# Performance work log

Hardware: AMD Instinct MI355X
Metric: run time of the kernel (lower is better)

Reference implementation:

```python
import jax, jax.numpy as jnp
import numpy as np

N_HEAD = 16
N_KV_HEAD = 4
HEAD_DIM = 64
ROPE_THETA = 10000.0
EPS = 1e-6


def _rope_cos_sin(T, D, theta):
    # matches torch: freqs_cis[t, i] = exp(1j * t * theta**(-2i/D)), i in [0, D//2)
    inv_freq = theta ** (-jnp.arange(0, D, 2, dtype=jnp.float32) / D)  # [D//2]
    freqs = jnp.arange(T, dtype=jnp.float32)[:, None] * inv_freq[None, :]  # [T, D//2]
    return jnp.cos(freqs), jnp.sin(freqs)


def _apply_rope(x, cos, sin):
    # x: [B, T, H, D]; pairs are (even, odd) along last dim, complex-multiplied by freqs_cis
    B, T, H, D = x.shape
    xr = x.reshape(B, T, H, D // 2, 2)
    xe, xo = xr[..., 0], xr[..., 1]
    c = cos[None, :, None, :]  # [1, T, 1, D//2]
    s = sin[None, :, None, :]
    oe = xe * c - xo * s
    oo = xe * s + xo * c
    return jnp.stack([oe, oo], axis=-1).reshape(B, T, H, D)


def _qk_norm(x):
    rms = jnp.sqrt(jnp.mean(x * x, axis=-1, keepdims=True) + EPS)
    return x / rms


def setup_inputs() -> dict:
    key = jax.random.key(0)
    k = jax.random.split(key, 5)
    B, T, C = 4, 2048, 1024
    sc = 1.0 / np.sqrt(C)
    return {
        "x": jax.random.normal(k[0], (B, T, C), jnp.float32),
        "wq": jax.random.normal(k[1], (N_HEAD * HEAD_DIM, C), jnp.float32) * sc,
        "wk": jax.random.normal(k[2], (N_KV_HEAD * HEAD_DIM, C), jnp.float32) * sc,
        "wv": jax.random.normal(k[3], (N_KV_HEAD * HEAD_DIM, C), jnp.float32) * sc,
        "wo": jax.random.normal(k[4], (C, N_HEAD * HEAD_DIM), jnp.float32) * sc,
    }


def reference(x, wq, wk, wv, wo):
    B, T, C = x.shape
    H, KVH, D = N_HEAD, N_KV_HEAD, HEAD_DIM
    n_rep = H // KVH

    q = (x @ wq.T).reshape(B, T, H, D)
    k = (x @ wk.T).reshape(B, T, KVH, D)
    v = (x @ wv.T).reshape(B, T, KVH, D)

    cos, sin = _rope_cos_sin(T, D, ROPE_THETA)
    q = _qk_norm(_apply_rope(q, cos, sin))
    k = _qk_norm(_apply_rope(k, cos, sin))

    # GQA expand kv heads to n_head
    k = jnp.repeat(k, n_rep, axis=2)  # [B, T, H, D]
    v = jnp.repeat(v, n_rep, axis=2)

    q = q.transpose(0, 2, 1, 3)  # [B, H, T, D]
    k = k.transpose(0, 2, 1, 3)
    v = v.transpose(0, 2, 1, 3)

    scale = 1.0 / np.sqrt(D)
    scores = jnp.einsum("bhqd,bhkd->bhqk", q, k) * scale
    causal = jnp.tril(jnp.ones((T, T), dtype=bool))
    scores = jnp.where(causal[None, None], scores, -jnp.inf)
    attn = jax.nn.softmax(scores, axis=-1)
    y = jnp.einsum("bhqk,bhkd->bhqd", attn, v)  # [B, H, T, D]
    y = y.transpose(0, 2, 1, 3).reshape(B, T, H * D)
    return y @ wo.T
```

## Files before the change

kernel.cpp:

```cpp
#include <hip/hip_runtime.h>
#include <hip/hip_bf16.h>
#include <type_traits>

typedef __attribute__((ext_vector_type(8))) __bf16 bf16x8;
typedef __attribute__((ext_vector_type(2))) float f32x2;
typedef __attribute__((ext_vector_type(4))) float f32x4;
typedef __attribute__((ext_vector_type(16))) float f32x16;

#define MFMA16(a, b, c) __builtin_amdgcn_mfma_f32_16x16x32_bf16((a), (b), (c), 0, 0, 0)
#define MFMA32(a, b, c) __builtin_amdgcn_mfma_f32_32x32x16_bf16((a), (b), (c), 0, 0, 0)

__device__ __forceinline__ unsigned short f2bf(float f) {
    unsigned u = __builtin_bit_cast(unsigned, f);
    u = (u + 0x7fffu + ((u >> 16) & 1u)) >> 16;
    return (unsigned short)u;
}

__device__ __forceinline__ float bf2f(unsigned short u) {
    return __builtin_bit_cast(float, (unsigned)u << 16);
}

__device__ __forceinline__ unsigned cvt_pk_bf16(float lo, float hi) {
    unsigned r;
    asm("v_cvt_pk_bf16_f32 %0, %1, %2" : "=v"(r) : "v"(lo), "v"(hi));
    return r;
}

__device__ __forceinline__ void permswap(unsigned& a, unsigned& b) {
    asm("v_permlane32_swap_b32 %0, %1" : "+v"(a), "+v"(b));
}

__device__ __forceinline__ void gll16(const void* g, void* l) {
    __builtin_amdgcn_global_load_lds((const __attribute__((address_space(1))) void*)g,
                                     (__attribute__((address_space(3))) void*)l, 16, 0, 0);
}

__global__ __launch_bounds__(256) void cvt_fused(const float4* __restrict__ x,
                                                 const float4* __restrict__ wq,
                                                 const float4* __restrict__ wk,
                                                 const float4* __restrict__ wv,
                                                 const float4* __restrict__ wo,
                                                 ushort4* __restrict__ xb,
                                                 ushort4* __restrict__ wqkvb,
                                                 ushort4* __restrict__ wob,
                                                 float2* __restrict__ tbl) {
    int i = blockIdx.x * 256 + threadIdx.x;
    if (i < 2752512) {
        const float4* src; ushort4* dst; int j;
        if (i < 2097152)      { src = x;  dst = xb;             j = i; }
        else if (i < 2359296) { src = wq; dst = wqkvb;          j = i - 2097152; }
        else if (i < 2424832) { src = wk; dst = wqkvb + 262144; j = i - 2359296; }
        else if (i < 2490368) { src = wv; dst = wqkvb + 327680; j = i - 2424832; }
        else                  { src = wo; dst = wob;            j = i - 2490368; }
        float4 v = src[j];
        ushort4 o;
        o.x = f2bf(v.x); o.y = f2bf(v.y); o.z = f2bf(v.z); o.w = f2bf(v.w);
        dst[j] = o;
    } else {
        int j = i - 2752512;
        int t = j >> 5, k = j & 31;
        float inv = powf(10000.0f, -(float)(2 * k) * (1.0f / 64.0f));
        float a = (float)t * inv;
        tbl[j] = make_float2(cosf(a), sinf(a));
    }
}

__global__ __launch_bounds__(256) void gemm_qkv(const unsigned short* __restrict__ A,
                                                const unsigned short* __restrict__ Bt,
                                                const float2* __restrict__ tbl,
                                                unsigned short* __restrict__ qb,
                                                unsigned short* __restrict__ kb,
                                                unsigned short* __restrict__ vt) {
    const int K = 1024;
    __shared__ unsigned short As[2][128 * 32];
    __shared__ unsigned short Bs[2][128 * 32];
    const int tid = threadIdx.x;
    const int wid = tid >> 6, lane = tid & 63;
    const size_t brow = (size_t)blockIdx.x * 128, bcol = (size_t)blockIdx.y * 128;
    const int nkt = K >> 5;

    auto stage = [&](int buf, int kt) {
#pragma unroll
        for (int j = 0; j < 2; ++j) {
            int e = (j * 256 + tid) * 8;
            int r = e >> 5, c = e & 31;
            gll16(A + (brow + r) * K + kt * 32 + c, &As[buf][e]);
        }
#pragma unroll
        for (int j = 0; j < 2; ++j) {
            int e = (j * 256 + tid) * 8;
            int r = e >> 5, c = e & 31;
            gll16(Bt + (bcol + r) * K + kt * 32 + c, &Bs[buf][e]);
        }
    };

    f32x4 acc[4][4] = {};
    const int wm = (wid >> 1) * 64, wn = (wid & 1) * 64;
    const int fr = lane & 15, fk = (lane >> 4) * 8;

    stage(0, 0);
    for (int kt = 0; kt < nkt; ++kt) {
        __syncthreads();
        if (kt + 1 < nkt) stage((kt + 1) & 1, kt + 1);
        const int buf = kt & 1;
        bf16x8 af[4], bfr[4];
#pragma unroll
        for (int i = 0; i < 4; ++i)
            af[i] = *(const bf16x8*)&As[buf][(wm + i * 16 + fr) * 32 + fk];
#pragma unroll
        for (int i = 0; i < 4; ++i)
            bfr[i] = *(const bf16x8*)&Bs[buf][(wn + i * 16 + fr) * 32 + fk];
#pragma unroll
        for (int i = 0; i < 4; ++i)
#pragma unroll
            for (int j = 0; j < 4; ++j)
                acc[i][j] = MFMA16(af[i], bfr[j], acc[i][j]);
    }

    const int orow = (lane >> 4) * 4, ocol = lane & 15;
    const int tokrow0 = (int)brow + wm;
    const int hcol0 = (int)bcol + wn;

    if (blockIdx.y < 10) {
        float ss[4][4];
#pragma unroll
        for (int i = 0; i < 4; ++i)
#pragma unroll
            for (int r = 0; r < 4; ++r) ss[i][r] = 0.0f;
#pragma unroll
        for (int i = 0; i < 4; ++i)
#pragma unroll
            for (int j = 0; j < 4; ++j) {
                const int m = (j * 16 + ocol) >> 1;
#pragma unroll
                for (int r = 0; r < 4; ++r) {
                    float xv = acc[i][j][r];
                    float partner = __shfl_xor(xv, 1);
                    int t = (tokrow0 + i * 16 + orow + r) & 2047;
                    float2 cs = tbl[t * 32 + m];
                    float sgn = (ocol & 1) ? cs.y : -cs.y;
                    float v = fmaf(xv, cs.x, partner * sgn);
                    acc[i][j][r] = v;
                    ss[i][r] += v * v;
                }
            }
#pragma unroll
        for (int off = 1; off < 16; off <<= 1)
#pragma unroll
            for (int i = 0; i < 4; ++i)
#pragma unroll
                for (int r = 0; r < 4; ++r) ss[i][r] += __shfl_xor(ss[i][r], off);
        const bool isq = (blockIdx.y < 8);
        const float qsc = isq ? 0.18033688f : 1.0f;
        const int h = hcol0 >> 6;
#pragma unroll
        for (int i = 0; i < 4; ++i)
#pragma unroll
            for (int r = 0; r < 4; ++r) {
                float sc = rsqrtf(ss[i][r] * (1.0f / 64.0f) + 1e-6f) * qsc;
                int grow = tokrow0 + i * 16 + orow + r;
                int b = grow >> 11, t = grow & 2047;
                unsigned short* dst = isq
                    ? qb + (((size_t)(b * 16 + h)) * 2048 + t) * 64
                    : kb + (((size_t)(b * 4 + (h - 16))) * 2048 + t) * 64;
#pragma unroll
                for (int j = 0; j < 4; ++j)
                    dst[j * 16 + ocol] = f2bf(acc[i][j][r] * sc);
            }
    } else {
#pragma unroll
        for (int j = 0; j < 4; ++j) {
            int vcol = (hcol0 - 1280) + j * 16 + ocol;
            int kvh = vcol >> 6, d = vcol & 63;
#pragma unroll
            for (int i = 0; i < 4; ++i) {
                int grow = tokrow0 + i * 16 + orow;
                int b = grow >> 11, t = grow & 2047;
                ushort4 w;
#pragma unroll
                for (int r = 0; r < 4; ++r)
                    ((unsigned short*)&w)[r] = f2bf(acc[i][j][r]);
                *(ushort4*)&vt[((size_t)(b * 4 + kvh) * 64 + d) * 2048 + t] = w;
            }
        }
    }
}

template <typename OT>
__global__ __launch_bounds__(256) void gemm_bt_t(const unsigned short* __restrict__ A,
                                                 const unsigned short* __restrict__ Bt,
                                                 OT* __restrict__ C, int M, int N, int K) {
    __shared__ unsigned short As[2][128 * 32];
    __shared__ unsigned short Bs[2][128 * 32];
    const int tid = threadIdx.x;
    const int wid = tid >> 6, lane = tid & 63;
    const size_t brow = (size_t)blockIdx.x * 128, bcol = (size_t)blockIdx.y * 128;
    const int nkt = K >> 5;

    auto stage = [&](int buf, int kt) {
#pragma unroll
        for (int j = 0; j < 2; ++j) {
            int e = (j * 256 + tid) * 8;
            int r = e >> 5, c = e & 31;
            gll16(A + (brow + r) * K + kt * 32 + c, &As[buf][e]);
        }
#pragma unroll
        for (int j = 0; j < 2; ++j) {
            int e = (j * 256 + tid) * 8;
            int r = e >> 5, c = e & 31;
            gll16(Bt + (bcol + r) * K + kt * 32 + c, &Bs[buf][e]);
        }
    };

    f32x4 acc[4][4] = {};
    const int wm = (wid >> 1) * 64, wn = (wid & 1) * 64;
    const int fr = lane & 15, fk = (lane >> 4) * 8;

    stage(0, 0);
    for (int kt = 0; kt < nkt; ++kt) {
        __syncthreads();
        if (kt + 1 < nkt) stage((kt + 1) & 1, kt + 1);
        const int buf = kt & 1;
        bf16x8 af[4], bfr[4];
#pragma unroll
        for (int i = 0; i < 4; ++i)
            af[i] = *(const bf16x8*)&As[buf][(wm + i * 16 + fr) * 32 + fk];
#pragma unroll
        for (int i = 0; i < 4; ++i)
            bfr[i] = *(const bf16x8*)&Bs[buf][(wn + i * 16 + fr) * 32 + fk];
#pragma unroll
        for (int i = 0; i < 4; ++i)
#pragma unroll
            for (int j = 0; j < 4; ++j)
                acc[i][j] = MFMA16(af[i], bfr[j], acc[i][j]);
    }

    const int orow = (lane >> 4) * 4, ocol = lane & 15;
#pragma unroll
    for (int i = 0; i < 4; ++i)
#pragma unroll
        for (int j = 0; j < 4; ++j)
#pragma unroll
            for (int r = 0; r < 4; ++r) {
                size_t idx = (brow + wm + i * 16 + orow + r) * N + (bcol + wn + j * 16 + ocol);
                if constexpr (std::is_same_v<OT, unsigned short>)
                    C[idx] = f2bf(acc[i][j][r]);
                else
                    C[idx] = acc[i][j][r];
            }
}

__global__ __launch_bounds__(256, 4) void attn_fwd(const unsigned short* __restrict__ qb,
                                                   const unsigned short* __restrict__ kbuf,
                                                   const unsigned short* __restrict__ vt,
                                                   unsigned short* __restrict__ Pp,
                                                   float* __restrict__ Lp) {
    int orig = blockIdx.x;
    int wg = (orig & 7) * 320 + (orig >> 3);
    int bh = wg / 40;
    int u = 39 - (wg - bh * 40);
    int qt, ci, nc;
    if (u < 4)       { qt = u;               ci = 0;            nc = 1; }
    else if (u < 12) { qt = 4 + ((u - 4) >> 1);  ci = (u - 4) & 1;  nc = 2; }
    else if (u < 24) { qt = 8 + (u - 12) / 3;    ci = (u - 12) % 3; nc = 3; }
    else             { qt = 12 + ((u - 24) >> 2); ci = (u - 24) & 3; nc = 4; }
    const int nkt = 2 * qt + 2;
    const int t0 = ci * nkt / nc, t1 = (ci + 1) * nkt / nc;
    const int qbase = qt * 128;

    int b = bh >> 4, h = bh & 15, kvh = h >> 2;
    int tid = threadIdx.x, wid = tid >> 6, lane = tid & 63;
    int qrow0 = qbase + wid * 32;
    const unsigned short* Q = qb + ((size_t)(b * 16 + h)) * 2048 * 64;
    const unsigned short* Kp = kbuf + ((size_t)(b * 4 + kvh)) * 2048 * 64;
    const unsigned short* Vp = vt + ((size_t)(b * 4 + kvh)) * 64 * 2048;
    const int q32 = lane & 31, hi = lane >> 5;
    const int swz = (q32 & 7) ^ ((q32 >> 3) & 3);

    __shared__ unsigned short Klds[2][4096];
    __shared__ unsigned short Vlds[2][4096];

    const unsigned short *gk0, *gk1, *gv0, *gv1;
    {
        int t = tid, k = t >> 3, c = (t & 7) ^ (k & 7) ^ ((k >> 3) & 3);
        gk0 = Kp + ((size_t)(t0 * 64 + k)) * 64 + c * 8;
        t = 256 + tid; k = t >> 3; c = (t & 7) ^ (k & 7) ^ ((k >> 3) & 3);
        gk1 = Kp + ((size_t)(t0 * 64 + k)) * 64 + c * 8;
        t = tid; int d = t >> 3; c = (t & 7) ^ (d & 7) ^ ((d >> 3) & 3);
        gv0 = Vp + (size_t)d * 2048 + t0 * 64 + c * 8;
        t = 256 + tid; d = t >> 3; c = (t & 7) ^ (d & 7) ^ ((d >> 3) & 3);
        gv1 = Vp + (size_t)d * 2048 + t0 * 64 + c * 8;
    }
    auto stage = [&](int buf) {
        gll16(gk0, &Klds[buf][tid * 8]);        gk0 += 4096;
        gll16(gk1, &Klds[buf][2048 + tid * 8]); gk1 += 4096;
        gll16(gv0, &Vlds[buf][tid * 8]);        gv0 += 64;
        gll16(gv1, &Vlds[buf][2048 + tid * 8]); gv1 += 64;
    };

    bf16x8 qf[4];
#pragma unroll
    for (int kd = 0; kd < 4; ++kd)
        qf[kd] = *(const bf16x8*)&Q[(qrow0 + q32) * 64 + kd * 16 + hi * 8];

    f32x16 accO[2] = {};
    f32x2 lra = {0.0f, 0.0f}, lrb = {0.0f, 0.0f}, lrc = {0.0f, 0.0f}, lrd = {0.0f, 0.0f};
    f32x16 s0v;
#pragma unroll
    for (int i = 0; i < 16; ++i) s0v[i] = -11.54156036f;

    stage(0);
    for (int kt = t0; kt < t1; ++kt) {
        __syncthreads();
        if (kt + 1 < t1) stage((kt + 1 - t0) & 1);
        const int cur = (kt - t0) & 1;
        const int kb0 = kt * 64;
        if (kb0 <= qrow0 + 31) {
            const int qg = qrow0 + q32;
            const bool diag = (kb0 + 63 > qrow0);
            bf16x8 pf[4];
#pragma unroll
            for (int j = 0; j < 2; ++j) {
                f32x16 s = s0v;
                const int row = j * 32 + q32;
                __builtin_amdgcn_s_setprio(1);
#pragma unroll
                for (int kd = 0; kd < 4; ++kd) {
                    bf16x8 kf = *(const bf16x8*)&Klds[cur][row * 64 + ((2 * kd + hi) ^ swz) * 8];
                    s = MFMA32(kf, qf[kd], s);
                }
                __builtin_amdgcn_s_setprio(0);
                float p[16];
                if (diag) {
#pragma unroll
                    for (int r = 0; r < 16; ++r) {
                        float v = __builtin_exp2f(s[r]);
                        int key = kb0 + j * 32 + (r & 3) + 8 * (r >> 2) + 4 * hi;
                        if (key > qg) v = 0.0f;
                        p[r] = v;
                    }
                } else {
#pragma unroll
                    for (int r = 0; r < 16; ++r) p[r] = __builtin_exp2f(s[r]);
                }
                {
                    f32x2 p0 = {p[0], p[1]},  p1 = {p[2], p[3]};
                    f32x2 p2 = {p[4], p[5]},  p3 = {p[6], p[7]};
                    asm("v_pk_add_f32 %0, %0, %1" : "+v"(lra) : "v"(p0));
                    asm("v_pk_add_f32 %0, %0, %1" : "+v"(lrb) : "v"(p1));
                    asm("v_pk_add_f32 %0, %0, %1" : "+v"(lrc) : "v"(p2));
                    asm("v_pk_add_f32 %0, %0, %1" : "+v"(lrd) : "v"(p3));
                    f32x2 p4 = {p[8], p[9]},  p5 = {p[10], p[11]};
                    f32x2 p6 = {p[12], p[13]}, p7 = {p[14], p[15]};
                    asm("v_pk_add_f32 %0, %0, %1" : "+v"(lra) : "v"(p4));
                    asm("v_pk_add_f32 %0, %0, %1" : "+v"(lrb) : "v"(p5));
                    asm("v_pk_add_f32 %0, %0, %1" : "+v"(lrc) : "v"(p6));
                    asm("v_pk_add_f32 %0, %0, %1" : "+v"(lrd) : "v"(p7));
                }
#pragma unroll
                for (int kl = 0; kl < 2; ++kl) {
                    unsigned c0 = cvt_pk_bf16(p[8 * kl + 0], p[8 * kl + 1]);
                    unsigned c1 = cvt_pk_bf16(p[8 * kl + 4], p[8 * kl + 5]);
                    unsigned c2 = cvt_pk_bf16(p[8 * kl + 2], p[8 * kl + 3]);
                    unsigned c3 = cvt_pk_bf16(p[8 * kl + 6], p[8 * kl + 7]);
                    permswap(c0, c1);
                    permswap(c2, c3);
                    union { bf16x8 v; unsigned u[4]; } pk;
                    pk.u[0] = c0; pk.u[1] = c2; pk.u[2] = c1; pk.u[3] = c3;
                    pf[j * 2 + kl] = pk.v;
                }
            }
            __builtin_amdgcn_s_setprio(1);
#pragma unroll
            for (int nd = 0; nd < 2; ++nd) {
                int row = nd * 32 + q32;
#pragma unroll
                for (int ks = 0; ks < 4; ++ks) {
                    bf16x8 vf = *(const bf16x8*)&Vlds[cur][row * 64 + ((2 * ks + hi) ^ swz) * 8];
                    accO[nd] = MFMA32(pf[ks], vf, accO[nd]);
                }
            }
            __builtin_amdgcn_s_setprio(0);
        }
    }

    asm("v_pk_add_f32 %0, %0, %1" : "+v"(lra) : "v"(lrc));
    asm("v_pk_add_f32 %0, %0, %1" : "+v"(lrb) : "v"(lrd));
    asm("v_pk_add_f32 %0, %0, %1" : "+v"(lra) : "v"(lrb));
    float lrun = lra[0] + lra[1];
    unsigned lu = __builtin_bit_cast(unsigned, lrun);
    unsigned la = lu, lb = lu;
    permswap(la, lb);
    float L = __builtin_bit_cast(float, la) + __builtin_bit_cast(float, lb);

    unsigned short* Pw = Pp + (((size_t)bh * 40 + u) * 128 + wid * 32) * 64;
#pragma unroll
    for (int nd = 0; nd < 2; ++nd)
#pragma unroll
        for (int r = 0; r < 16; ++r) {
            int lrow = (r & 3) + 8 * (r >> 2) + 4 * hi;
            Pw[(size_t)lrow * 64 + nd * 32 + q32] = f2bf(accO[nd][r]);
        }
    if (lane < 32)
        Lp[((size_t)bh * 40 + u) * 128 + wid * 32 + q32] = L;
}

__global__ __launch_bounds__(256) void attn_fin(const unsigned short* __restrict__ Pp,
                                                const float* __restrict__ Lp,
                                                unsigned short* __restrict__ y) {
    int idx = blockIdx.x * 256 + threadIdx.x;
    int dg = idx & 15;
    int grow = idx >> 4;
    int bh = grow >> 11, t = grow & 2047;
    int b = bh >> 4, h = bh & 15;
    int qt = t >> 7;
    int bse, nc;
    if (qt < 4)       { bse = qt;                nc = 1; }
    else if (qt < 8)  { bse = 4 + 2 * (qt - 4);  nc = 2; }
    else if (qt < 12) { bse = 12 + 3 * (qt - 8); nc = 3; }
    else              { bse = 24 + 4 * (qt - 12); nc = 4; }
    float o0 = 0.f, o1 = 0.f, o2 = 0.f, o3 = 0.f, L = 0.f;
    for (int ci = 0; ci < nc; ++ci) {
        size_t slot = ((size_t)bh * 40 + bse + ci) * 128 + (t & 127);
        ushort4 pw = *(const ushort4*)&Pp[slot * 64 + dg * 4];
        o0 += bf2f(pw.x); o1 += bf2f(pw.y); o2 += bf2f(pw.z); o3 += bf2f(pw.w);
        L += Lp[slot];
    }
    float inv = 1.0f / L;
    ushort4 w;
    w.x = f2bf(o0 * inv); w.y = f2bf(o1 * inv);
    w.z = f2bf(o2 * inv); w.w = f2bf(o3 * inv);
    *(ushort4*)&y[((size_t)(b * 2048 + t)) * 1024 + h * 64 + dg * 4] = w;
}

extern "C" void kernel_launch(void* const* d_in, const int* in_sizes, int n_in,
                              void* d_out, int out_size, void* d_ws, size_t ws_size,
                              hipStream_t stream) {
    const float* x = (const float*)d_in[0];
    const float* wq = (const float*)d_in[1];
    const float* wk = (const float*)d_in[2];
    const float* wv = (const float*)d_in[3];
    const float* wo = (const float*)d_in[4];
    float* out = (float*)d_out;

    char* ws = (char*)d_ws;
    size_t off = 0;
    auto alloc = [&](size_t bytes) {
        void* p = ws + off;
        off += (bytes + 255) & ~(size_t)255;
        return p;
    };
    unsigned short* xb    = (unsigned short*)alloc(8192ull * 1024 * 2);
    unsigned short* wqkvb = (unsigned short*)alloc(1536ull * 1024 * 2);
    unsigned short* wob   = (unsigned short*)alloc(1024ull * 1024 * 2);
    unsigned short* Pp    = (unsigned short*)alloc(41943040ull);
    float*          Lp    = (float*)alloc(1310720ull);
    float2*         tbl   = (float2*)alloc(2048ull * 32 * 8);
    unsigned short* qb    = (unsigned short*)alloc(8192ull * 1024 * 2);
    unsigned short* kb    = (unsigned short*)alloc(4ull * 4 * 2048 * 64 * 2);
    unsigned short* vt    = (unsigned short*)alloc(4ull * 4 * 64 * 2048 * 2);
    unsigned short* ybf   = xb;

    cvt_fused<<<11008, 256, 0, stream>>>((const float4*)x, (const float4*)wq, (const float4*)wk,
                                         (const float4*)wv, (const float4*)wo,
                                         (ushort4*)xb, (ushort4*)wqkvb, (ushort4*)wob, tbl);

    gemm_qkv<<<dim3(64, 12), 256, 0, stream>>>(xb, wqkvb, tbl, qb, kb, vt);

    attn_fwd<<<2560, 256, 0, stream>>>(qb, kb, vt, Pp, Lp);

    attn_fin<<<8192, 256, 0, stream>>>(Pp, Lp, ybf);

    gemm_bt_t<float><<<dim3(64, 8), 256, 0, stream>>>(ybf, wob, out, 8192, 1024, 1024);
}
```

Before: 174.2 us.

## Load K/V fragments directly from global memory instead of LDS double-buffering

Removes the shared-memory double-buffered staging of K and V tiles along with the per-iteration __syncthreads. Each wave now reads its K and V MFMA fragments straight from global memory (relying on L1/L2 caching). The loop bound is clipped per wave to the causal limit, so the inner causal branch is dropped. The cost is that the four waves share each tile through cache instead of loading it once into LDS, and global latency is no longer hidden by the async prefetch.

Measured after the change: 291.1 us. 67.1% more time.

```diff
diff --git a/kernel.cpp b/kernel.cpp
--- a/kernel.cpp
+++ b/kernel.cpp
@@ -275,28 +275,6 @@
     const unsigned short* Kp = kbuf + ((size_t)(b * 4 + kvh)) * 2048 * 64;
     const unsigned short* Vp = vt + ((size_t)(b * 4 + kvh)) * 64 * 2048;
     const int q32 = lane & 31, hi = lane >> 5;
-    const int swz = (q32 & 7) ^ ((q32 >> 3) & 3);
-
-    __shared__ unsigned short Klds[2][4096];
-    __shared__ unsigned short Vlds[2][4096];
-
-    const unsigned short *gk0, *gk1, *gv0, *gv1;
-    {
-        int t = tid, k = t >> 3, c = (t & 7) ^ (k & 7) ^ ((k >> 3) & 3);
-        gk0 = Kp + ((size_t)(t0 * 64 + k)) * 64 + c * 8;
-        t = 256 + tid; k = t >> 3; c = (t & 7) ^ (k & 7) ^ ((k >> 3) & 3);
-        gk1 = Kp + ((size_t)(t0 * 64 + k)) * 64 + c * 8;
-        t = tid; int d = t >> 3; c = (t & 7) ^ (d & 7) ^ ((d >> 3) & 3);
-        gv0 = Vp + (size_t)d * 2048 + t0 * 64 + c * 8;
-        t = 256 + tid; d = t >> 3; c = (t & 7) ^ (d & 7) ^ ((d >> 3) & 3);
-        gv1 = Vp + (size_t)d * 2048 + t0 * 64 + c * 8;
-    }
-    auto stage = [&](int buf) {
-        gll16(gk0, &Klds[buf][tid * 8]);        gk0 += 4096;
-        gll16(gk1, &Klds[buf][2048 + tid * 8]); gk1 += 4096;
-        gll16(gv0, &Vlds[buf][tid * 8]);        gv0 += 64;
-        gll16(gv1, &Vlds[buf][2048 + tid * 8]); gv1 += 64;
-    };
 
     bf16x8 qf[4];
 #pragma unroll
@@ -309,79 +287,74 @@
 #pragma unroll
     for (int i = 0; i < 16; ++i) s0v[i] = -11.54156036f;
 
-    stage(0);
-    for (int kt = t0; kt < t1; ++kt) {
-        __syncthreads();
-        if (kt + 1 < t1) stage((kt + 1 - t0) & 1);
-        const int cur = (kt - t0) & 1;
+    const int tEnd = min(t1, ((qrow0 + 31) >> 6) + 1);
+    for (int kt = t0; kt < tEnd; ++kt) {
         const int kb0 = kt * 64;
-        if (kb0 <= qrow0 + 31) {
-            const int qg = qrow0 + q32;
-            const bool diag = (kb0 + 63 > qrow0);
-            bf16x8 pf[4];
-#pragma unroll
-            for (int j = 0; j < 2; ++j) {
-                f32x16 s = s0v;
-                const int row = j * 32 + q32;
-                __builtin_amdgcn_s_setprio(1);
-#pragma unroll
-                for (int kd = 0; kd < 4; ++kd) {
-                    bf16x8 kf = *(const bf16x8*)&Klds[cur][row * 64 + ((2 * kd + hi) ^ swz) * 8];
-                    s = MFMA32(kf, qf[kd], s);
+        const int qg = qrow0 + q32;
+        const bool diag = (kb0 + 63 > qrow0);
+        bf16x8 pf[4];
+#pragma unroll
+        for (int j = 0; j < 2; ++j) {
+            f32x16 s = s0v;
+            const int krow = kb0 + j * 32 + q32;
+            __builtin_amdgcn_s_setprio(1);
+#pragma unroll
+            for (int kd = 0; kd < 4; ++kd) {
+                bf16x8 kf = *(const bf16x8*)&Kp[(size_t)krow * 64 + kd * 16 + hi * 8];
+                s = MFMA32(kf, qf[kd], s);
+            }
+            __builtin_amdgcn_s_setprio(0);
+            float p[16];
+            if (diag) {
+#pragma unroll
+                for (int r = 0; r < 16; ++r) {
+                    float v = __builtin_exp2f(s[r]);
+                    int key = kb0 + j * 32 + (r & 3) + 8 * (r >> 2) + 4 * hi;
+                    if (key > qg) v = 0.0f;
+                    p[r] = v;
                 }
-                __builtin_amdgcn_s_setprio(0);
-                float p[16];
-                if (diag) {
-#pragma unroll
-                    for (int r = 0; r < 16; ++r) {
-                        float v = __builtin_exp2f(s[r]);
-                        int key = kb0 + j * 32 + (r & 3) + 8 * (r >> 2) + 4 * hi;
-                        if (key > qg) v = 0.0f;
-                        p[r] = v;
-                    }
-                } else {
-#pragma unroll
-                    for (int r = 0; r < 16; ++r) p[r] = __builtin_exp2f(s[r]);
-                }
-                {
-                    f32x2 p0 = {p[0], p[1]},  p1 = {p[2], p[3]};
-                    f32x2 p2 = {p[4], p[5]},  p3 = {p[6], p[7]};
-                    asm("v_pk_add_f32 %0, %0, %1" : "+v"(lra) : "v"(p0));
-                    asm("v_pk_add_f32 %0, %0, %1" : "+v"(lrb) : "v"(p1));
-                    asm("v_pk_add_f32 %0, %0, %1" : "+v"(lrc) : "v"(p2));
-                    asm("v_pk_add_f32 %0, %0, %1" : "+v"(lrd) : "v"(p3));
-                    f32x2 p4 = {p[8], p[9]},  p5 = {p[10], p[11]};
-                    f32x2 p6 = {p[12], p[13]}, p7 = {p[14], p[15]};
-                    asm("v_pk_add_f32 %0, %0, %1" : "+v"(lra) : "v"(p4));
-                    asm("v_pk_add_f32 %0, %0, %1" : "+v"(lrb) : "v"(p5));
-                    asm("v_pk_add_f32 %0, %0, %1" : "+v"(lrc) : "v"(p6));
-                    asm("v_pk_add_f32 %0, %0, %1" : "+v"(lrd) : "v"(p7));
-                }
-#pragma unroll
-                for (int kl = 0; kl < 2; ++kl) {
-                    unsigned c0 = cvt_pk_bf16(p[8 * kl + 0], p[8 * kl + 1]);
-                    unsigned c1 = cvt_pk_bf16(p[8 * kl + 4], p[8 * kl + 5]);
-                    unsigned c2 = cvt_pk_bf16(p[8 * kl + 2], p[8 * kl + 3]);
-                    unsigned c3 = cvt_pk_bf16(p[8 * kl + 6], p[8 * kl + 7]);
-                    permswap(c0, c1);
-                    permswap(c2, c3);
-                    union { bf16x8 v; unsigned u[4]; } pk;
-                    pk.u[0] = c0; pk.u[1] = c2; pk.u[2] = c1; pk.u[3] = c3;
-                    pf[j * 2 + kl] = pk.v;
-                }
-            }
-            __builtin_amdgcn_s_setprio(1);
-#pragma unroll
-            for (int nd = 0; nd < 2; ++nd) {
-                int row = nd * 32 + q32;
-#pragma unroll
-                for (int ks = 0; ks < 4; ++ks) {
-                    bf16x8 vf = *(const bf16x8*)&Vlds[cur][row * 64 + ((2 * ks + hi) ^ swz) * 8];
-                    accO[nd] = MFMA32(pf[ks], vf, accO[nd]);
-                }
-            }
-            __builtin_amdgcn_s_setprio(0);
-        }
+            } else {
+#pragma unroll
+                for (int r = 0; r < 16; ++r) p[r] = __builtin_exp2f(s[r]);
+            }
+            {
+                f32x2 p0 = {p[0], p[1]},  p1 = {p[2], p[3]};
+                f32x2 p2 = {p[4], p[5]},  p3 = {p[6], p[7]};
+                asm("v_pk_add_f32 %0, %0, %1" : "+v"(lra) : "v"(p0));
+                asm("v_pk_add_f32 %0, %0, %1" : "+v"(lrb) : "v"(p1));
+                asm("v_pk_add_f32 %0, %0, %1" : "+v"(lrc) : "v"(p2));
+                asm("v_pk_add_f32 %0, %0, %1" : "+v"(lrd) : "v"(p3));
+                f32x2 p4 = {p[8], p[9]},  p5 = {p[10], p[11]};
+                f32x2 p6 = {p[12], p[13]}, p7 = {p[14], p[15]};
+                asm("v_pk_add_f32 %0, %0, %1" : "+v"(lra) : "v"(p4));
+                asm("v_pk_add_f32 %0, %0, %1" : "+v"(lrb) : "v"(p5));
+                asm("v_pk_add_f32 %0, %0, %1" : "+v"(lrc) : "v"(p6));
+                asm("v_pk_add_f32 %0, %0, %1" : "+v"(lrd) : "v"(p7));
+            }
+#pragma unroll
+            for (int kl = 0; kl < 2; ++kl) {
+                unsigned c0 = cvt_pk_bf16(p[8 * kl + 0], p[8 * kl + 1]);
+                unsigned c1 = cvt_pk_bf16(p[8 * kl + 4], p[8 * kl + 5]);
+                unsigned c2 = cvt_pk_bf16(p[8 * kl + 2], p[8 * kl + 3]);
+                unsigned c3 = cvt_pk_bf16(p[8 * kl + 6], p[8 * kl + 7]);
+                permswap(c0, c1);
+                permswap(c2, c3);
+                union { bf16x8 v; unsigned u[4]; } pk;
+                pk.u[0] = c0; pk.u[1] = c2; pk.u[2] = c1; pk.u[3] = c3;
+                pf[j * 2 + kl] = pk.v;
+            }
+        }
+        __builtin_amdgcn_s_setprio(1);
+#pragma unroll
+        for (int nd = 0; nd < 2; ++nd) {
+            int vrow = nd * 32 + q32;
+#pragma unroll
+            for (int ks = 0; ks < 4; ++ks) {
+                bf16x8 vf = *(const bf16x8*)&Vp[(size_t)vrow * 2048 + kb0 + ks * 16 + hi * 8];
+                accO[nd] = MFMA32(pf[ks], vf, accO[nd]);
+            }
+        }
+        __builtin_amdgcn_s_setprio(0);
     }
 
     asm("v_pk_add_f32 %0, %0, %1" : "+v"(lra) : "v"(lrc));
```
